# Performance work log

Hardware: AMD Instinct MI355X
Metric: run time of the kernel (lower is better)

The kernel has to match this reference:

```python
import jax, jax.numpy as jnp
import numpy as np

B, S, N, D, H = 4, 2048, 2048, 1024, 16
HD = D // H  # 64
EPS = 1e-5


def layer_norm(x, w, b):
    m = x.mean(axis=-1, keepdims=True)
    v = ((x - m) ** 2).mean(axis=-1, keepdims=True)
    return (x - m) / jnp.sqrt(v + EPS) * w + b


def setup_inputs() -> dict:
    key = jax.random.key(0)
    ks = jax.random.split(key, 4)
    x_q = jax.random.normal(ks[0], (B, S, D), dtype=jnp.float32)
    x_k = jax.random.normal(ks[1], (B, N, HD), dtype=jnp.float32)
    x_v = jax.random.normal(ks[2], (B, N, HD), dtype=jnp.float32)
    # learned params
    qn_w = jnp.ones((HD,), jnp.float32)
    qn_b = jnp.zeros((HD,), jnp.float32)
    kn_w = jnp.ones((HD,), jnp.float32)
    kn_b = jnp.zeros((HD,), jnp.float32)
    n_w = jnp.ones((D,), jnp.float32)
    n_b = jnp.zeros((D,), jnp.float32)
    # xavier-uniform proj weight (D, D), no bias (proj_bias=False)
    limit = np.sqrt(6.0 / (D + D))
    proj_w = jax.random.uniform(ks[3], (D, D), jnp.float32, -limit, limit)
    return {"x_q": x_q, "x_k": x_k, "x_v": x_v,
            "qn_w": qn_w, "qn_b": qn_b, "kn_w": kn_w, "kn_b": kn_b,
            "n_w": n_w, "n_b": n_b, "proj_w": proj_w}


def reference(x_q, x_k, x_v, qn_w, qn_b, kn_w, kn_b, n_w, n_b, proj_w):
    scale = HD ** -0.5
    # faithful to torch: q.reshape(B, H, -1, head_dim) -- NO transpose before reshape
    q = x_q.reshape(B, H, S, HD)
    q = layer_norm(q, qn_w, qn_b)
    k = layer_norm(x_k, kn_w, kn_b)
    q = q * scale
    attn = jnp.einsum('bhsd,bnd->bhsn', q, k)  # (B,H,S,N) shared K across heads
    attn = jax.nn.softmax(attn, axis=-1)
    x = jnp.einsum('bhsn,bnd->bhsd', attn, x_v)  # shared V across heads
    x = jnp.transpose(x, (0, 2, 1, 3)).reshape(B, S, D)
    x = layer_norm(x, n_w, n_b)
    x = x @ proj_w.T  # nn.Linear: x W^T
    return x
```

## Files before the change

### kernel.cpp

```cpp
#include <hip/hip_runtime.h>

#define B_ 4
#define S_ 2048
#define N_ 2048
#define H_ 16
#define D_ 1024

typedef short s4v __attribute__((ext_vector_type(4)));
typedef short s8v __attribute__((ext_vector_type(8)));
typedef float f4v __attribute__((ext_vector_type(4)));

__device__ __forceinline__ float bf2f(short s) {
  unsigned u = ((unsigned)(unsigned short)s) << 16;
  float f; __builtin_memcpy(&f, &u, 4); return f;
}
__device__ __forceinline__ short f2bf(float f) {
  unsigned u; __builtin_memcpy(&u, &f, 4);
  u += 0x7fffu + ((u >> 16) & 1u);
  return (short)(u >> 16);
}
__device__ __forceinline__ unsigned pack2bf(float a, float b) {
  unsigned ua, ub;
  __builtin_memcpy(&ua, &a, 4);
  __builtin_memcpy(&ub, &b, 4);
  return __builtin_amdgcn_perm(ub + 0x8000u, ua + 0x8000u, 0x07060302u);
}
__device__ __forceinline__ unsigned pk2(float a, float b) {
  unsigned ua, ub;
  __builtin_memcpy(&ua, &a, 4);
  __builtin_memcpy(&ub, &b, 4);
  return __builtin_amdgcn_perm(ub, ua, 0x07060302u);
}
__device__ __forceinline__ s8v load8f32(const float* p) {
  const f4v* q = (const f4v*)p;
  f4v a = q[0], b = q[1];
  union { s8v v; unsigned u[4]; } o;
  o.u[0] = pack2bf(a[0], a[1]); o.u[1] = pack2bf(a[2], a[3]);
  o.u[2] = pack2bf(b[0], b[1]); o.u[3] = pack2bf(b[2], b[3]);
  return o.v;
}
__device__ __forceinline__ void gld16(const char* g, char* l) {
  __builtin_amdgcn_global_load_lds(
      (const __attribute__((address_space(1))) unsigned*)g,
      (__attribute__((address_space(3))) unsigned*)l, 16, 0, 0);
}

__global__ __launch_bounds__(256) void prep_kernel(
    const float* __restrict__ xk, const float* __restrict__ knw,
    const float* __restrict__ knb, short* __restrict__ kws,
    const float* __restrict__ xv, short* __restrict__ vtp) {
  __shared__ __align__(16) short vstage[4][2048];
  int blk = blockIdx.x;
  if (blk < 2048) {
    int gid = blk * 256 + threadIdx.x;
    int row = gid >> 6, lane = gid & 63;
    float v = xk[(size_t)row * 64 + lane];
    float s = v;
    #pragma unroll
    for (int mm = 1; mm < 64; mm <<= 1) s += __shfl_xor(s, mm, 64);
    float mean = s * 0.015625f;
    float d = v - mean;
    float vs = d * d;
    #pragma unroll
    for (int mm = 1; mm < 64; mm <<= 1) vs += __shfl_xor(vs, mm, 64);
    float rstd = rsqrtf(vs * 0.015625f + 1e-5f);
    kws[(size_t)row * 72 + lane] = f2bf(d * rstd * knw[lane] + knb[lane]);
  } else {
    int wave = threadIdx.x >> 6, lane = threadIdx.x & 63;
    int u = (blk - 2048) * 4 + wave;
    int b = u >> 6, nb = u & 63;
    int r = lane >> 1, dh = lane & 1;
    const float* src = xv + ((size_t)(b * N_ + nb * 32 + r)) * 64 + dh * 32;
    int qq = (r & 15) >> 2;
    int slot = ((r >> 4) << 2) + (r & 3);
    short* wbase = &vstage[wave][0];
    #pragma unroll
    for (int jj = 0; jj < 32; jj += 4) {
      f4v f = *(const f4v*)(src + jj);
      #pragma unroll
      for (int e = 0; e < 4; e++) {
        int d = dh * 32 + jj + e;
        wbase[d * 32 + qq * 8 + slot] = f2bf(f[e]);
      }
    }
    __syncthreads();
    s8v* dst = (s8v*)(vtp + (size_t)u * 2560 + lane * 40);
    const s8v* sp = (const s8v*)(wbase + lane * 32);
    dst[0] = sp[0]; dst[1] = sp[1]; dst[2] = sp[2]; dst[3] = sp[3];
  }
}

__global__ __launch_bounds__(256, 4) void flash_kernel(
    const float* __restrict__ xq, const float* __restrict__ qnw,
    const float* __restrict__ qnb, const short* __restrict__ kws,
    const short* __restrict__ vtp, short* __restrict__ aout) {
  __shared__ __align__(16) union {
    char qs[128 * 144];
    struct { char k[2][9216]; char v[2][10240]; } kv;
  } lds;
  int blk = blockIdx.x;
  int sblk = blk & 15, bh = blk >> 4, b = bh >> 4;
  int t = threadIdx.x, wave = t >> 6, lane = t & 63;
  int m = lane & 15, q = lane >> 4;
  const float QSCALE = 0.125f * 1.4426950408889634f;

  const char* kb = (const char*)kws + (size_t)b * N_ * 144;
  const char* vb = (const char*)vtp + (size_t)b * 64 * 5120;

  gld16(vb + t * 16,        lds.kv.v[0] + t * 16);
  gld16(vb + 4096 + t * 16, lds.kv.v[0] + 4096 + t * 16);
  if (t < 128) gld16(vb + 8192 + t * 16, lds.kv.v[0] + 8192 + t * 16);

  {
    int r = t >> 1, half = t & 1;
    const float* qr = xq + ((size_t)bh * S_ + sblk * 128 + r) * 64 + half * 32;
    f4v f[8];
    float s = 0.f, ss = 0.f;
    #pragma unroll
    for (int i = 0; i < 8; i++) {
      f[i] = *(const f4v*)(qr + i * 4);
      s += (f[i][0] + f[i][1]) + (f[i][2] + f[i][3]);
      ss += (f[i][0] * f[i][0] + f[i][1] * f[i][1]) + (f[i][2] * f[i][2] + f[i][3] * f[i][3]);
    }
    s += __shfl_xor(s, 1, 64);
    ss += __shfl_xor(ss, 1, 64);
    float mean = s * 0.015625f;
    float rstd = rsqrtf(ss * 0.015625f - mean * mean + 1e-5f);
    #pragma unroll
    for (int i = 0; i < 4; i++) {
      float y[8];
      #pragma unroll
      for (int e = 0; e < 4; e++) {
        int gi = half * 32 + i * 8;
        y[e]     = ((f[2 * i][e]     - mean) * rstd * qnw[gi + e]     + qnb[gi + e])     * QSCALE;
        y[4 + e] = ((f[2 * i + 1][e] - mean) * rstd * qnw[gi + 4 + e] + qnb[gi + 4 + e]) * QSCALE;
      }
      union { s8v v; unsigned u[4]; } o8;
      #pragma unroll
      for (int e = 0; e < 4; e++) o8.u[e] = pack2bf(y[2 * e], y[2 * e + 1]);
      *(s8v*)(lds.qs + r * 144 + half * 64 + i * 16) = o8.v;
    }
  }
  __syncthreads();

  s8v qlo[2], qhi[2];
  #pragma unroll
  for (int mt = 0; mt < 2; mt++) {
    const char* qrow = lds.qs + (wave * 32 + mt * 16 + m) * 144;
    qlo[mt] = *(const s8v*)(qrow + q * 16);
    qhi[mt] = *(const s8v*)(qrow + 64 + q * 16);
  }
  __syncthreads();

  gld16(kb + t * 16,        lds.kv.k[0] + t * 16);
  gld16(kb + 4096 + t * 16, lds.kv.k[0] + 4096 + t * 16);
  if (t < 64) gld16(kb + 8192 + t * 16, lds.kv.k[0] + 8192 + t * 16);
  __syncthreads();

  f4v zero4 = {0.f, 0.f, 0.f, 0.f};
  f4v o[2][4], lacc[2];
  #pragma unroll
  for (int mt = 0; mt < 2; mt++) {
    lacc[mt] = zero4;
    #pragma unroll
    for (int tt = 0; tt < 4; tt++) o[mt][tt] = zero4;
  }
  s8v ones;
  #pragma unroll
  for (int e = 0; e < 8; e++) ones[e] = (short)0x3F80;

  for (int it = 0; it < 32; ++it) {
    int cur = it & 1;
    if (it < 31) {
      const char* kg = kb + (size_t)(it + 1) * 9216;
      const char* vg = vb + (size_t)(it + 1) * 10240;
      char* kd = lds.kv.k[cur ^ 1];
      char* vd = lds.kv.v[cur ^ 1];
      gld16(kg + t * 16,        kd + t * 16);
      gld16(kg + 4096 + t * 16, kd + 4096 + t * 16);
      if (t < 64) gld16(kg + 8192 + t * 16, kd + 8192 + t * 16);
      gld16(vg + t * 16,        vd + t * 16);
      gld16(vg + 4096 + t * 16, vd + 4096 + t * 16);
      if (t < 128) gld16(vg + 8192 + t * 16, vd + 8192 + t * 16);
    }
    const char* kc = lds.kv.k[cur];
    const char* vc = lds.kv.v[cur];

    #pragma unroll
    for (int g = 0; g < 2; g++) {
      s8v a0lo = *(const s8v*)(kc + (g * 32 + m) * 144 + q * 16);
      s8v a0hi = *(const s8v*)(kc + (g * 32 + m) * 144 + 64 + q * 16);
      s8v a1lo = *(const s8v*)(kc + (g * 32 + 16 + m) * 144 + q * 16);
      s8v a1hi = *(const s8v*)(kc + (g * 32 + 16 + m) * 144 + 64 + q * 16);
      s8v vf[4];
      #pragma unroll
      for (int tt = 0; tt < 4; tt++)
        vf[tt] = *(const s8v*)(vc + g * 5120 + (tt * 16 + m) * 80 + q * 16);

      #pragma unroll
      for (int mt = 0; mt < 2; mt++) {
        f4v s0 = zero4, s1 = zero4;
        s0 = __builtin_amdgcn_mfma_f32_16x16x32_bf16(a0lo, qlo[mt], s0, 0, 0, 0);
        s0 = __builtin_amdgcn_mfma_f32_16x16x32_bf16(a0hi, qhi[mt], s0, 0, 0, 0);
        s1 = __builtin_amdgcn_mfma_f32_16x16x32_bf16(a1lo, qlo[mt], s1, 0, 0, 0);
        s1 = __builtin_amdgcn_mfma_f32_16x16x32_bf16(a1hi, qhi[mt], s1, 0, 0, 0);
        float p[8];
        #pragma unroll
        for (int i = 0; i < 4; i++) {
          p[i]     = __builtin_amdgcn_exp2f(s0[i]);
          p[4 + i] = __builtin_amdgcn_exp2f(s1[i]);
        }
        union { s8v v; unsigned u[4]; } pa;
        #pragma unroll
        for (int i = 0; i < 4; i++) pa.u[i] = pk2(p[2 * i], p[2 * i + 1]);
        lacc[mt] = __builtin_amdgcn_mfma_f32_16x16x32_bf16(pa.v, ones, lacc[mt], 0, 0, 0);
        #pragma unroll
        for (int tt = 0; tt < 4; tt++)
          o[mt][tt] = __builtin_amdgcn_mfma_f32_16x16x32_bf16(pa.v, vf[tt], o[mt][tt], 0, 0, 0);
      }
    }
    __syncthreads();
  }

  #pragma unroll
  for (int mt = 0; mt < 2; mt++) {
    #pragma unroll
    for (int i = 0; i < 4; i++) {
      float inv = __builtin_amdgcn_rcpf(lacc[mt][i]);
      int srow = sblk * 128 + wave * 32 + mt * 16 + q * 4 + i;
      size_t orow = ((size_t)b * S_ + srow) * D_ + (size_t)(bh & 15) * 64;
      #pragma unroll
      for (int tt = 0; tt < 4; tt++)
        aout[orow + tt * 16 + m] = f2bf(o[mt][tt][i] * inv);
    }
  }
}

__global__ __launch_bounds__(256) void ln_d_kernel(
    const short* __restrict__ x, const float* __restrict__ w,
    const float* __restrict__ bb, short* __restrict__ y) {
  int row = blockIdx.x * 4 + (threadIdx.x >> 6);
  int lane = threadIdx.x & 63;
  const short* xr = x + (size_t)row * D_ + lane * 16;
  s8v v0 = *(const s8v*)xr;
  s8v v1 = *(const s8v*)(xr + 8);
  float f[16];
  #pragma unroll
  for (int e = 0; e < 8; e++) { f[e] = bf2f(v0[e]); f[8 + e] = bf2f(v1[e]); }
  float s = 0.f, ss = 0.f;
  #pragma unroll
  for (int e = 0; e < 16; e++) { s += f[e]; ss += f[e] * f[e]; }
  #pragma unroll
  for (int mm = 1; mm < 64; mm <<= 1) {
    s += __shfl_xor(s, mm, 64);
    ss += __shfl_xor(ss, mm, 64);
  }
  float mean = s * (1.0f / 1024.0f);
  float rstd = rsqrtf(ss * (1.0f / 1024.0f) - mean * mean + 1e-5f);
  const float* wp = w + lane * 16;
  const float* bp = bb + lane * 16;
  union { s8v v[2]; short sh[16]; } o;
  #pragma unroll
  for (int e = 0; e < 16; e++)
    o.sh[e] = f2bf((f[e] - mean) * rstd * wp[e] + bp[e]);
  short* yr = y + (size_t)row * D_ + lane * 16;
  *(s8v*)yr = o.v[0];
  *(s8v*)(yr + 8) = o.v[1];
}

__global__ __launch_bounds__(256, 2) void proj_gemm(
    const short* __restrict__ A, const float* __restrict__ Bw,
    float* __restrict__ C) {
  __shared__ __align__(16) char la[2][16384];
  __shared__ __align__(16) char lb[2][16384];
  int wg = (blockIdx.x & 7) * 64 + (blockIdx.x >> 3);
  int bm = (wg >> 3) * 128;
  int bn = (wg & 7) * 128;
  int t = threadIdx.x, wave = t >> 6, lane = t & 63;
  int m = lane & 15, q = lane >> 4;
  int wm = (wave & 1) * 64, wn = (wave >> 1) * 64;

  int arow0 = t >> 3, au = t & 7;
  const char* abase = (const char*)(A + (size_t)bm * 1024);
  int brow = t >> 1, bu0 = (t & 1) * 4;
  const float* bwbase = Bw + (size_t)(bn + brow) * 1024;
  char* lbrow0 = lb[0] + brow * 128;
  char* lbrow1 = lb[1] + brow * 128;

  f4v zero4 = {0.f, 0.f, 0.f, 0.f};
  f4v acc[4][4];
  #pragma unroll
  for (int i = 0; i < 4; i++)
    #pragma unroll
    for (int j = 0; j < 4; j++) acc[i][j] = zero4;

  #pragma unroll
  for (int c = 0; c < 4; c++) {
    int row = c * 32 + arow0;
    gld16(abase + (size_t)row * 2048 + (size_t)(au ^ (row & 7)) * 16,
          la[0] + c * 4096 + t * 16);
  }
  #pragma unroll
  for (int j = 0; j < 4; j++) {
    int u = bu0 + j;
    s8v bv = load8f32(bwbase + u * 8);
    *(s8v*)(lbrow0 + ((u ^ (brow & 7)) * 16)) = bv;
  }
  __syncthreads();

  for (int it = 0; it < 16; ++it) {
    int cur = it & 1;
    if (it < 15) {
      int k0 = (it + 1) * 64;
      char* ad = la[cur ^ 1];
      char* bd = (cur ^ 1) ? lbrow1 : lbrow0;
      #pragma unroll
      for (int c = 0; c < 4; c++) {
        int row = c * 32 + arow0;
        gld16(abase + (size_t)row * 2048 + (size_t)k0 * 2 +
                  (size_t)(au ^ (row & 7)) * 16,
              ad + c * 4096 + t * 16);
      }
      #pragma unroll
      for (int j = 0; j < 4; j++) {
        int u = bu0 + j;
        s8v bv = load8f32(bwbase + k0 + u * 8);
        *(s8v*)(bd + ((u ^ (brow & 7)) * 16)) = bv;
      }
    }
    const char* lac = la[cur];
    const char* lbc = lb[cur];
    #pragma unroll
    for (int kh = 0; kh < 2; kh++) {
      s8v af[4], bfv[4];
      #pragma unroll
      for (int i = 0; i < 4; i++) {
        int r = wm + i * 16 + m;
        af[i] = *(const s8v*)(lac + r * 128 + (((kh * 4 + q) ^ (r & 7)) * 16));
      }
      #pragma unroll
      for (int j = 0; j < 4; j++) {
        int r = wn + j * 16 + m;
        bfv[j] = *(const s8v*)(lbc + r * 128 + (((kh * 4 + q) ^ (r & 7)) * 16));
      }
      #pragma unroll
      for (int i = 0; i < 4; i++)
        #pragma unroll
        for (int j = 0; j < 4; j++)
          acc[i][j] = __builtin_amdgcn_mfma_f32_16x16x32_bf16(af[i], bfv[j], acc[i][j], 0, 0, 0);
    }
    __syncthreads();
  }

  #pragma unroll
  for (int i = 0; i < 4; i++)
    #pragma unroll
    for (int j = 0; j < 4; j++)
      #pragma unroll
      for (int r = 0; r < 4; r++) {
        int row = bm + wm + i * 16 + q * 4 + r;
        int col = bn + wn + j * 16 + m;
        C[(size_t)row * 1024 + col] = acc[i][j][r];
      }
}

extern "C" void kernel_launch(void* const* d_in, const int* in_sizes, int n_in,
                              void* d_out, int out_size, void* d_ws, size_t ws_size,
                              hipStream_t stream) {
  const float* xq  = (const float*)d_in[0];
  const float* xk  = (const float*)d_in[1];
  const float* xv  = (const float*)d_in[2];
  const float* qnw = (const float*)d_in[3];
  const float* qnb = (const float*)d_in[4];
  const float* knw = (const float*)d_in[5];
  const float* knb = (const float*)d_in[6];
  const float* nw  = (const float*)d_in[7];
  const float* nb  = (const float*)d_in[8];
  const float* pw  = (const float*)d_in[9];
  float* out = (float*)d_out;

  short* kws = (short*)d_ws;
  short* vtp = (short*)((char*)d_ws + 0x120000);
  short* yws = (short*)d_ws;
  short* aout = (short*)d_out;

  prep_kernel<<<2112, 256, 0, stream>>>(xk, knw, knb, kws, xv, vtp);
  flash_kernel<<<1024, 256, 0, stream>>>(xq, qnw, qnb, kws, vtp, aout);
  ln_d_kernel<<<B_ * S_ / 4, 256, 0, stream>>>(aout, nw, nb, yws);
  proj_gemm<<<512, 256, 0, stream>>>(yws, pw, out);
}
```

Baseline: 219.1 us.

## Fold LayerNorm affine into projection weights and apply row stats in GEMM epilogue

The final LayerNorm is split algebraically. Gamma is folded into a bf16 copy of the projection weight, and the per-column sums of gamma*W and beta*W are precomputed in the prep kernel. A small stats kernel now only writes per-row rstd and -mean*rstd. The GEMM reads the raw attention output and the pre-converted bf16 weights through global_load_lds, then applies the row stats and column terms in the epilogue. This removes the normalized intermediate write/read and the fp32-to-bf16 weight conversion inside the GEMM, at the cost of a larger workspace and of normalizing after the bf16 product, which changes rounding.

Measured after the change: 201.5 us. -8.0%, faster.

```diff
diff --git a/kernel.cpp b/kernel.cpp
--- a/kernel.cpp
+++ b/kernel.cpp
@@ -9,6 +9,7 @@
 typedef short s4v __attribute__((ext_vector_type(4)));
 typedef short s8v __attribute__((ext_vector_type(8)));
 typedef float f4v __attribute__((ext_vector_type(4)));
+typedef float f2v __attribute__((ext_vector_type(2)));
 
 __device__ __forceinline__ float bf2f(short s) {
   unsigned u = ((unsigned)(unsigned short)s) << 16;
@@ -48,7 +49,10 @@
 __global__ __launch_bounds__(256) void prep_kernel(
     const float* __restrict__ xk, const float* __restrict__ knw,
     const float* __restrict__ knb, short* __restrict__ kws,
-    const float* __restrict__ xv, short* __restrict__ vtp) {
+    const float* __restrict__ xv, short* __restrict__ vtp,
+    const float* __restrict__ pw, const float* __restrict__ nw_,
+    const float* __restrict__ nb_, short* __restrict__ wpb,
+    float* __restrict__ t12) {
   __shared__ __align__(16) short vstage[4][2048];
   int blk = blockIdx.x;
   if (blk < 2048) {
@@ -65,7 +69,7 @@
     for (int mm = 1; mm < 64; mm <<= 1) vs += __shfl_xor(vs, mm, 64);
     float rstd = rsqrtf(vs * 0.015625f + 1e-5f);
     kws[(size_t)row * 72 + lane] = f2bf(d * rstd * knw[lane] + knb[lane]);
-  } else {
+  } else if (blk < 2112) {
     int wave = threadIdx.x >> 6, lane = threadIdx.x & 63;
     int u = (blk - 2048) * 4 + wave;
     int b = u >> 6, nb = u & 63;
@@ -87,6 +91,39 @@
     s8v* dst = (s8v*)(vtp + (size_t)u * 2560 + lane * 40);
     const s8v* sp = (const s8v*)(wbase + lane * 32);
     dst[0] = sp[0]; dst[1] = sp[1]; dst[2] = sp[2]; dst[3] = sp[3];
+  } else {
+    int jr = threadIdx.x >> 4;
+    int lc = (threadIdx.x & 15) * 64;
+    int j = (blk - 2112) * 16 + jr;
+    const float* wr = pw + (size_t)j * 1024 + lc;
+    float t1p = 0.f, t2p = 0.f;
+    #pragma unroll
+    for (int c = 0; c < 64; c += 8) {
+      f4v w0 = *(const f4v*)(wr + c);
+      f4v w1 = *(const f4v*)(wr + c + 4);
+      f4v g0 = *(const f4v*)(nw_ + lc + c);
+      f4v g1 = *(const f4v*)(nw_ + lc + c + 4);
+      f4v b0 = *(const f4v*)(nb_ + lc + c);
+      f4v b1 = *(const f4v*)(nb_ + lc + c + 4);
+      float p[8];
+      #pragma unroll
+      for (int e = 0; e < 4; e++) {
+        p[e]     = g0[e] * w0[e];
+        p[4 + e] = g1[e] * w1[e];
+        t1p += p[e] + p[4 + e];
+        t2p += b0[e] * w0[e] + b1[e] * w1[e];
+      }
+      union { s8v v; unsigned u[4]; } o8;
+      o8.u[0] = pack2bf(p[0], p[1]); o8.u[1] = pack2bf(p[2], p[3]);
+      o8.u[2] = pack2bf(p[4], p[5]); o8.u[3] = pack2bf(p[6], p[7]);
+      *(s8v*)(wpb + (size_t)j * 1024 + lc + c) = o8.v;
+    }
+    #pragma unroll
+    for (int mm = 1; mm < 16; mm <<= 1) {
+      t1p += __shfl_xor(t1p, mm, 64);
+      t2p += __shfl_xor(t2p, mm, 64);
+    }
+    if ((threadIdx.x & 15) == 0) { t12[j * 2] = t1p; t12[j * 2 + 1] = t2p; }
   }
 }
 
@@ -268,7 +305,33 @@
   *(s8v*)(yr + 8) = o.v[1];
 }
 
-__global__ __launch_bounds__(256, 2) void proj_gemm(
+__global__ __launch_bounds__(256) void stats_kernel(
+    const short* __restrict__ x, float* __restrict__ st) {
+  int row = blockIdx.x * 4 + (threadIdx.x >> 6);
+  int lane = threadIdx.x & 63;
+  const short* xr = x + (size_t)row * D_ + lane * 16;
+  s8v v0 = *(const s8v*)xr;
+  s8v v1 = *(const s8v*)(xr + 8);
+  float s = 0.f, ss = 0.f;
+  #pragma unroll
+  for (int e = 0; e < 8; e++) {
+    float a = bf2f(v0[e]), b = bf2f(v1[e]);
+    s += a + b; ss += a * a + b * b;
+  }
+  #pragma unroll
+  for (int mm = 1; mm < 64; mm <<= 1) {
+    s += __shfl_xor(s, mm, 64);
+    ss += __shfl_xor(ss, mm, 64);
+  }
+  if (lane == 0) {
+    float mean = s * (1.0f / 1024.0f);
+    float rstd = rsqrtf(ss * (1.0f / 1024.0f) - mean * mean + 1e-5f);
+    f2v o = {rstd, -mean * rstd};
+    *(f2v*)(st + (size_t)row * 2) = o;
+  }
+}
+
+__global__ __launch_bounds__(256, 2) void proj_gemm_fb(
     const short* __restrict__ A, const float* __restrict__ Bw,
     float* __restrict__ C) {
   __shared__ __align__(16) char la[2][16384];
@@ -362,6 +425,95 @@
         int col = bn + wn + j * 16 + m;
         C[(size_t)row * 1024 + col] = acc[i][j][r];
       }
+}
+
+__global__ __launch_bounds__(256, 2) void proj_gemm_fx(
+    const short* __restrict__ A, const short* __restrict__ Wp,
+    const float* __restrict__ t12, const float* __restrict__ st,
+    float* __restrict__ C) {
+  __shared__ __align__(16) char la[2][16384];
+  __shared__ __align__(16) char lb[2][16384];
+  int wg = (blockIdx.x & 7) * 64 + (blockIdx.x >> 3);
+  int bm = (wg >> 3) * 128;
+  int bn = (wg & 7) * 128;
+  int t = threadIdx.x, wave = t >> 6, lane = t & 63;
+  int m = lane & 15, q = lane >> 4;
+  int wm = (wave & 1) * 64, wn = (wave >> 1) * 64;
+
+  int arow0 = t >> 3, au = t & 7;
+  const char* abase = (const char*)(A + (size_t)bm * 1024);
+  const char* bbase = (const char*)(Wp + (size_t)bn * 1024);
+
+  f4v zero4 = {0.f, 0.f, 0.f, 0.f};
+  f4v acc[4][4];
+  #pragma unroll
+  for (int i = 0; i < 4; i++)
+    #pragma unroll
+    for (int j = 0; j < 4; j++) acc[i][j] = zero4;
+
+  #pragma unroll
+  for (int c = 0; c < 4; c++) {
+    int row = c * 32 + arow0;
+    size_t so = (size_t)row * 2048 + (size_t)(au ^ (row & 7)) * 16;
+    gld16(abase + so, la[0] + c * 4096 + t * 16);
+    gld16(bbase + so, lb[0] + c * 4096 + t * 16);
+  }
+  __syncthreads();
+
+  for (int it = 0; it < 16; ++it) {
+    int cur = it & 1;
+    if (it < 15) {
+      int k0 = (it + 1) * 64;
+      #pragma unroll
+      for (int c = 0; c < 4; c++) {
+        int row = c * 32 + arow0;
+        size_t so = (size_t)row * 2048 + (size_t)k0 * 2 +
+                    (size_t)(au ^ (row & 7)) * 16;
+        gld16(abase + so, la[cur ^ 1] + c * 4096 + t * 16);
+        gld16(bbase + so, lb[cur ^ 1] + c * 4096 + t * 16);
+      }
+    }
+    const char* lac = la[cur];
+    const char* lbc = lb[cur];
+    #pragma unroll
+    for (int kh = 0; kh < 2; kh++) {
+      s8v af[4], bfv[4];
+      #pragma unroll
+      for (int i = 0; i < 4; i++) {
+        int r = wm + i * 16 + m;
+        af[i] = *(const s8v*)(lac + r * 128 + (((kh * 4 + q) ^ (r & 7)) * 16));
+      }
+      #pragma unroll
+      for (int j = 0; j < 4; j++) {
+        int r = wn + j * 16 + m;
+        bfv[j] = *(const s8v*)(lbc + r * 128 + (((kh * 4 + q) ^ (r & 7)) * 16));
+      }
+      #pragma unroll
+      for (int i = 0; i < 4; i++)
+        #pragma unroll
+        for (int j = 0; j < 4; j++)
+          acc[i][j] = __builtin_amdgcn_mfma_f32_16x16x32_bf16(af[i], bfv[j], acc[i][j], 0, 0, 0);
+    }
+    __syncthreads();
+  }
+
+  f2v tc[4];
+  #pragma unroll
+  for (int j = 0; j < 4; j++)
+    tc[j] = *(const f2v*)(t12 + (size_t)(bn + wn + j * 16 + m) * 2);
+  #pragma unroll
+  for (int i = 0; i < 4; i++)
+    #pragma unroll
+    for (int r = 0; r < 4; r++) {
+      int row = bm + wm + i * 16 + q * 4 + r;
+      f2v sr_ = *(const f2v*)(st + (size_t)row * 2);
+      #pragma unroll
+      for (int j = 0; j < 4; j++) {
+        int col = bn + wn + j * 16 + m;
+        C[(size_t)row * 1024 + col] =
+            sr_[0] * acc[i][j][r] + sr_[1] * tc[j][0] + tc[j][1];
+      }
+    }
 }
 
 extern "C" void kernel_launch(void* const* d_in, const int* in_sizes, int n_in,
@@ -379,13 +531,28 @@
   const float* pw  = (const float*)d_in[9];
   float* out = (float*)d_out;
 
-  short* kws = (short*)d_ws;
-  short* vtp = (short*)((char*)d_ws + 0x120000);
-  short* yws = (short*)d_ws;
-  short* aout = (short*)d_out;
-
-  prep_kernel<<<2112, 256, 0, stream>>>(xk, knw, knb, kws, xv, vtp);
-  flash_kernel<<<1024, 256, 0, stream>>>(xq, qnw, qnb, kws, vtp, aout);
-  ln_d_kernel<<<B_ * S_ / 4, 256, 0, stream>>>(aout, nw, nb, yws);
-  proj_gemm<<<512, 256, 0, stream>>>(yws, pw, out);
-}
+  const size_t NEED = 21438464;
+  if (ws_size >= NEED) {
+    short* aoutw = (short*)d_ws;
+    short* kws = (short*)((char*)d_ws + 16777216);
+    short* vtp = (short*)((char*)d_ws + 17956864);
+    short* wpb = (short*)((char*)d_ws + 19267584);
+    float* t12 = (float*)((char*)d_ws + 21364736);
+    float* st  = (float*)((char*)d_ws + 21372928);
+    prep_kernel<<<2176, 256, 0, stream>>>(xk, knw, knb, kws, xv, vtp,
+                                          pw, nw, nb, wpb, t12);
+    flash_kernel<<<1024, 256, 0, stream>>>(xq, qnw, qnb, kws, vtp, aoutw);
+    stats_kernel<<<2048, 256, 0, stream>>>(aoutw, st);
+    proj_gemm_fx<<<512, 256, 0, stream>>>(aoutw, wpb, t12, st, out);
+  } else {
+    short* kws = (short*)d_ws;
+    short* vtp = (short*)((char*)d_ws + 0x120000);
+    short* yws = (short*)d_ws;
+    short* aout = (short*)d_out;
+    prep_kernel<<<2112, 256, 0, stream>>>(xk, knw, knb, kws, xv, vtp,
+                                          pw, nw, nb, (short*)d_ws, (float*)d_ws);
+    flash_kernel<<<1024, 256, 0, stream>>>(xq, qnw, qnb, kws, vtp, aout);
+    ln_d_kernel<<<B_ * S_ / 4, 256, 0, stream>>>(aout, nw, nb, yws);
+    proj_gemm_fb<<<512, 256, 0, stream>>>(yws, pw, out);
+  }
+}
```
